# Optimization experiments

Hardware: AMD Instinct MI355X
Metric: run time of the kernel (lower is better)

## Reference

```python
import jax, jax.numpy as jnp
import numpy as np

N_NODES = 50000
N_EDGES = 800000
N_GRAPHS = 64
NEG_SLOPE = 0.2


def _gat_layer(x, src, dst, W, a_src, a_dst, b, heads, out_ch):
    """PyG-style GATConv (concat=True, eval mode, self loops already in src/dst)."""
    N = x.shape[0]
    h = (x @ W).reshape(N, heads, out_ch)                 # [N,H,C]
    al_src = jnp.sum(h * a_src, axis=-1)                  # [N,H]
    al_dst = jnp.sum(h * a_dst, axis=-1)                  # [N,H]
    e = jax.nn.leaky_relu(al_src[src] + al_dst[dst], NEG_SLOPE)  # [E,H]
    m = jax.ops.segment_max(e, dst, num_segments=N)       # scatter-softmax (stable)
    e = jnp.exp(e - m[dst])
    s = jax.ops.segment_sum(e, dst, num_segments=N)
    alpha = e / (s[dst] + 1e-16)                          # [E,H]
    msg = h[src] * alpha[..., None]                       # [E,H,C]
    out = jax.ops.segment_sum(msg, dst, num_segments=N)   # [N,H,C]
    return out.reshape(N, heads * out_ch) + b


def setup_inputs() -> dict:
    key = jax.random.key(0)
    ks = jax.random.split(key, 20)
    x = jax.random.normal(ks[0], (N_NODES, 2), dtype=jnp.float32)
    edge_index = jax.random.randint(ks[1], (2, N_EDGES), 0, N_NODES, dtype=jnp.int64)
    batch = jnp.sort(jax.random.randint(ks[2], (N_NODES,), 0, N_GRAPHS, dtype=jnp.int64))

    def glorot(k, shape):
        fan = sum(shape)
        return jax.random.uniform(k, shape, jnp.float32, -1.0, 1.0) * jnp.sqrt(6.0 / fan)

    return {
        "x": x, "edge_index": edge_index, "batch": batch,
        # gat1: 2 -> 64, heads=2, concat -> 128
        "w1": glorot(ks[3], (2, 128)),
        "a_src1": glorot(ks[4], (2, 64)),
        "a_dst1": glorot(ks[5], (2, 64)),
        "b1": jnp.zeros((128,), jnp.float32),
        # gat2: 128 -> 64, heads=1
        "w2": glorot(ks[6], (128, 64)),
        "a_src2": glorot(ks[7], (1, 64)),
        "a_dst2": glorot(ks[8], (1, 64)),
        "b2": jnp.zeros((64,), jnp.float32),
        # gat3: 64 -> 64, heads=1
        "w3": glorot(ks[9], (64, 64)),
        "a_src3": glorot(ks[10], (1, 64)),
        "a_dst3": glorot(ks[11], (1, 64)),
        "b3": jnp.zeros((64,), jnp.float32),
        # MLP head
        "fw1": glorot(ks[12], (64, 32)),
        "fb1": jnp.zeros((32,), jnp.float32),
        "fw2": glorot(ks[13], (32, 1)),
        "fb2": jnp.zeros((1,), jnp.float32),
    }


def reference(x, edge_index, batch,
              w1, a_src1, a_dst1, b1,
              w2, a_src2, a_dst2, b2,
              w3, a_src3, a_dst3, b3,
              fw1, fb1, fw2, fb2):
    N = x.shape[0]
    loops = jnp.arange(N, dtype=edge_index.dtype)
    src = jnp.concatenate([edge_index[0], loops])  # add self loops (PyG default)
    dst = jnp.concatenate([edge_index[1], loops])

    h = jax.nn.elu(_gat_layer(x, src, dst, w1, a_src1, a_dst1, b1, heads=2, out_ch=64))
    h = jax.nn.elu(_gat_layer(h, src, dst, w2, a_src2, a_dst2, b2, heads=1, out_ch=64))
    h = jax.nn.elu(_gat_layer(h, src, dst, w3, a_src3, a_dst3, b3, heads=1, out_ch=64))

    # global mean pool
    sums = jax.ops.segment_sum(h, batch, num_segments=N_GRAPHS)          # [B,64]
    cnts = jax.ops.segment_sum(jnp.ones((N,), h.dtype), batch, num_segments=N_GRAPHS)
    g = sums / jnp.maximum(cnts, 1.0)[:, None]

    g = jax.nn.relu(g @ fw1 + fb1)
    return g @ fw2 + fb2
```

## Files before the change

kernel.cpp:

```cpp
#include <hip/hip_runtime.h>
#include <hip/hip_bf16.h>
#include <math.h>

#define NN 50000
#define NE 800000
#define ET 850000
#define NG 64
#define NBLK 196


__global__ void count_k(const int* __restrict__ ei, int* __restrict__ counts) {
    int e = blockIdx.x * blockDim.x + threadIdx.x;
    if (e >= ET) return;
    int dst = (e < NE) ? ei[NE + e] : (e - NE);
    atomicAdd(&counts[dst], 1);
}

__global__ __launch_bounds__(256) void scan1_k(const int* __restrict__ counts,
                                               int* __restrict__ offsets,
                                               int* __restrict__ bsum) {
    int t = threadIdx.x;
    int idx = blockIdx.x * 256 + t;
    int v = (idx < NN) ? counts[idx] : 0;
    int lane = t & 63, wave = t >> 6;
    int inc = v;
#pragma unroll
    for (int d = 1; d < 64; d <<= 1) {
        int u = __shfl_up(inc, d);
        if (lane >= d) inc += u;
    }
    __shared__ int wtot[4];
    if (lane == 63) wtot[wave] = inc;
    __syncthreads();
    int wpre = 0;
    for (int w = 0; w < wave; w++) wpre += wtot[w];
    if (idx < NN) offsets[idx] = wpre + inc - v;
    if (t == 255) bsum[blockIdx.x] = wpre + inc;
}

__global__ __launch_bounds__(256) void scan2_k(const int* __restrict__ bsum,
                                               int* __restrict__ bpre,
                                               int* __restrict__ offsets) {
    int t = threadIdx.x;
    int v = (t < NBLK) ? bsum[t] : 0;
    int lane = t & 63, wave = t >> 6;
    int inc = v;
#pragma unroll
    for (int d = 1; d < 64; d <<= 1) {
        int u = __shfl_up(inc, d);
        if (lane >= d) inc += u;
    }
    __shared__ int wtot[4];
    if (lane == 63) wtot[wave] = inc;
    __syncthreads();
    int wpre = 0;
    for (int w = 0; w < wave; w++) wpre += wtot[w];
    if (t < NBLK) bpre[t] = wpre + inc - v;
    if (t == 0) offsets[NN] = ET;
}

__global__ __launch_bounds__(256) void scan3_k(int* __restrict__ offsets,
                                               const int* __restrict__ bpre) {
    int idx = blockIdx.x * 256 + threadIdx.x;
    if (idx < NN) offsets[idx] += bpre[blockIdx.x];
}

__global__ void scatter_k(const int* __restrict__ ei, const int* __restrict__ offsets,
                          int* __restrict__ cursor, int* __restrict__ csr_src) {
    int e = blockIdx.x * blockDim.x + threadIdx.x;
    if (e >= ET) return;
    int src, dst;
    if (e < NE) { src = ei[e]; dst = ei[NE + e]; }
    else        { src = dst = e - NE; }
    int pos = offsets[dst] + atomicAdd(&cursor[dst], 1);
    csr_src[pos] = src;
}

__global__ __launch_bounds__(256) void sortw_k(const int* __restrict__ offsets,
                                               int* __restrict__ csr) {
    int gt = blockIdx.x * blockDim.x + threadIdx.x;
    int n = gt >> 6;
    int lane = gt & 63;
    if (n >= NN) return;
    int b0 = offsets[n], b1 = offsets[n + 1];
    int deg = b1 - b0;
    if (deg <= 1) return;
    if (deg <= 64) {
        int v = (lane < deg) ? csr[b0 + lane] : 0x7FFFFFFF;
#pragma unroll
        for (int k = 2; k <= 64; k <<= 1) {
#pragma unroll
            for (int j = k >> 1; j > 0; j >>= 1) {
                int partner = __shfl_xor(v, j);
                bool up = ((lane & k) == 0);
                bool keepmin = (((lane & j) == 0) == up);
                v = keepmin ? min(v, partner) : max(v, partner);
            }
        }
        if (lane < deg) csr[b0 + lane] = v;
    } else if (lane == 0) {
        for (int i = b0 + 1; i < b1; i++) {
            int v = csr[i];
            int j = i - 1;
            while (j >= b0 && csr[j] > v) { csr[j + 1] = csr[j]; j--; }
            csr[j + 1] = v;
        }
    }
}


__global__ __launch_bounds__(256) void feat1b_k(const float* __restrict__ x,
                                                const float* __restrict__ w1,
                                                const float* __restrict__ as1,
                                                const float* __restrict__ ad1,
                                                float* __restrict__ alS,
                                                float* __restrict__ alD) {
    int t = threadIdx.x;
    int tt = t & 127;
    int n = blockIdx.x * 2 + (t >> 7);
    float x0 = x[n * 2 + 0], x1 = x[n * 2 + 1];
    float v = x0 * w1[tt] + x1 * w1[128 + tt];
    int head = (t >> 6) & 1, lane = t & 63;
    float ps = v * as1[tt];
    float pd = v * ad1[tt];
    for (int d = 32; d; d >>= 1) {
        ps += __shfl_down(ps, d);
        pd += __shfl_down(pd, d);
    }
    if (lane == 0) {
        alS[n * 2 + head] = ps;
        alD[n * 2 + head] = pd;
    }
}


__global__ __launch_bounds__(256) void agg1_k(const float2* __restrict__ x2,
                                              const float* __restrict__ w1,
                                              const float* __restrict__ alS,
                                              const float* __restrict__ alD,
                                              const float* __restrict__ bias,
                                              const int* __restrict__ offsets,
                                              const int* __restrict__ csr,
                                              float* __restrict__ out) {
    __shared__ float4 wslds[4][64];
    int t = threadIdx.x;
    int wave = t >> 6, lane = t & 63, grp = lane >> 4, c4 = lane & 15;
    int gl = lane & 15;
    int n = blockIdx.x * 4 + wave;
    int b0 = offsets[n], b1 = offsets[n + 1];
    int deg = b1 - b0;
    float2 adv = ((const float2*)alD)[n];
    const float2* alS2 = (const float2*)alS;

    float4 wa0 = ((const float4*)w1)[c4];
    float4 wa1 = ((const float4*)w1)[16 + c4];
    float4 wb0 = ((const float4*)(w1 + 128))[c4];
    float4 wb1 = ((const float4*)(w1 + 128))[16 + c4];
    float4 acc0 = make_float4(0.f, 0.f, 0.f, 0.f);
    float4 acc1 = make_float4(0.f, 0.f, 0.f, 0.f);
    float inv0, inv1;

    if (deg <= 64) {
        bool valid = lane < deg;
        int s = 0; float ev0 = -1e30f, ev1 = -1e30f;
        if (valid) {
            s = csr[b0 + lane];
            float2 al = alS2[s];
            float e0 = al.x + adv.x;
            ev0 = e0 > 0.f ? e0 : 0.2f * e0;
            float e1 = al.y + adv.y;
            ev1 = e1 > 0.f ? e1 : 0.2f * e1;
        }
        float m0 = ev0, m1 = ev1;
#pragma unroll
        for (int d = 32; d; d >>= 1) {
            m0 = fmaxf(m0, __shfl_xor(m0, d));
            m1 = fmaxf(m1, __shfl_xor(m1, d));
        }
        if (valid) {
            float w0 = expf(ev0 - m0);
            float w1v = expf(ev1 - m1);
            wslds[wave][lane] = make_float4(w0, w1v, __int_as_float(s), 0.f);
        }
        float ssum0 = 0.f, ssum1 = 0.f;
#pragma unroll
        for (int k = 0; k < 4; k++) {
            int j = gl + 16 * k;
            if (j < deg) {
                float4 f = wslds[wave][j];
                ssum0 += f.x;
                ssum1 += f.y;
            }
        }
        for (int d = 8; d; d >>= 1) {
            ssum0 += __shfl_xor(ssum0, d);
            ssum1 += __shfl_xor(ssum1, d);
        }
        inv0 = 1.f / (ssum0 + 1e-16f);
        inv1 = 1.f / (ssum1 + 1e-16f);
        int j = grp;
        for (; j + 4 < deg; j += 8) {
            float4 fa = wslds[wave][j];
            float4 fb = wslds[wave][j + 4];
            float2 xa = x2[__float_as_int(fa.z)];
            float2 xb = x2[__float_as_int(fb.z)];
            float4 v0, v1;
            v0.x = xa.x * wa0.x + xa.y * wb0.x;
            v0.y = xa.x * wa0.y + xa.y * wb0.y;
            v0.z = xa.x * wa0.z + xa.y * wb0.z;
            v0.w = xa.x * wa0.w + xa.y * wb0.w;
            v1.x = xa.x * wa1.x + xa.y * wb1.x;
            v1.y = xa.x * wa1.y + xa.y * wb1.y;
            v1.z = xa.x * wa1.z + xa.y * wb1.z;
            v1.w = xa.x * wa1.w + xa.y * wb1.w;
            acc0.x = fmaf(fa.x, v0.x, acc0.x);
            acc0.y = fmaf(fa.x, v0.y, acc0.y);
            acc0.z = fmaf(fa.x, v0.z, acc0.z);
            acc0.w = fmaf(fa.x, v0.w, acc0.w);
            acc1.x = fmaf(fa.y, v1.x, acc1.x);
            acc1.y = fmaf(fa.y, v1.y, acc1.y);
            acc1.z = fmaf(fa.y, v1.z, acc1.z);
            acc1.w = fmaf(fa.y, v1.w, acc1.w);
            v0.x = xb.x * wa0.x + xb.y * wb0.x;
            v0.y = xb.x * wa0.y + xb.y * wb0.y;
            v0.z = xb.x * wa0.z + xb.y * wb0.z;
            v0.w = xb.x * wa0.w + xb.y * wb0.w;
            v1.x = xb.x * wa1.x + xb.y * wb1.x;
            v1.y = xb.x * wa1.y + xb.y * wb1.y;
            v1.z = xb.x * wa1.z + xb.y * wb1.z;
            v1.w = xb.x * wa1.w + xb.y * wb1.w;
            acc0.x = fmaf(fb.x, v0.x, acc0.x);
            acc0.y = fmaf(fb.x, v0.y, acc0.y);
            acc0.z = fmaf(fb.x, v0.z, acc0.z);
            acc0.w = fmaf(fb.x, v0.w, acc0.w);
            acc1.x = fmaf(fb.y, v1.x, acc1.x);
            acc1.y = fmaf(fb.y, v1.y, acc1.y);
            acc1.z = fmaf(fb.y, v1.z, acc1.z);
            acc1.w = fmaf(fb.y, v1.w, acc1.w);
        }
        if (j < deg) {
            float4 fa = wslds[wave][j];
            float2 xa = x2[__float_as_int(fa.z)];
            float4 v0, v1;
            v0.x = xa.x * wa0.x + xa.y * wb0.x;
            v0.y = xa.x * wa0.y + xa.y * wb0.y;
            v0.z = xa.x * wa0.z + xa.y * wb0.z;
            v0.w = xa.x * wa0.w + xa.y * wb0.w;
            v1.x = xa.x * wa1.x + xa.y * wb1.x;
            v1.y = xa.x * wa1.y + xa.y * wb1.y;
            v1.z = xa.x * wa1.z + xa.y * wb1.z;
            v1.w = xa.x * wa1.w + xa.y * wb1.w;
            acc0.x = fmaf(fa.x, v0.x, acc0.x);
            acc0.y = fmaf(fa.x, v0.y, acc0.y);
            acc0.z = fmaf(fa.x, v0.z, acc0.z);
            acc0.w = fmaf(fa.x, v0.w, acc0.w);
            acc1.x = fmaf(fa.y, v1.x, acc1.x);
            acc1.y = fmaf(fa.y, v1.y, acc1.y);
            acc1.z = fmaf(fa.y, v1.z, acc1.z);
            acc1.w = fmaf(fa.y, v1.w, acc1.w);
        }
    } else {
        for (int head = 0; head < 2; head++) {
            float ad = head ? adv.y : adv.x;
            float4 wa = head ? wa1 : wa0, wb = head ? wb1 : wb0;
            float m = -1e30f;
            for (int i = b0 + gl; i < b1; i += 16) {
                int s = csr[i];
                float ev = alS[s * 2 + head] + ad;
                ev = ev > 0.f ? ev : 0.2f * ev;
                m = fmaxf(m, ev);
            }
            for (int d = 8; d; d >>= 1) m = fmaxf(m, __shfl_xor(m, d));
            float ssum = 0.f;
            for (int i = b0 + gl; i < b1; i += 16) {
                int s = csr[i];
                float ev = alS[s * 2 + head] + ad;
                ev = ev > 0.f ? ev : 0.2f * ev;
                float w = expf(ev - m);
                ssum += w;
            }
            for (int d = 8; d; d >>= 1) ssum += __shfl_xor(ssum, d);
            float invh = 1.f / (ssum + 1e-16f);
            float4 acc = make_float4(0.f, 0.f, 0.f, 0.f);
            for (int i = b0 + grp; i < b1; i += 4) {
                int s = csr[i];
                float ev = alS[s * 2 + head] + ad;
                ev = ev > 0.f ? ev : 0.2f * ev;
                float w = expf(ev - m);
                float2 xs = x2[s];
                float4 v;
                v.x = xs.x * wa.x + xs.y * wb.x;
                v.y = xs.x * wa.y + xs.y * wb.y;
                v.z = xs.x * wa.z + xs.y * wb.z;
                v.w = xs.x * wa.w + xs.y * wb.w;
                acc.x = fmaf(w, v.x, acc.x);
                acc.y = fmaf(w, v.y, acc.y);
                acc.z = fmaf(w, v.z, acc.z);
                acc.w = fmaf(w, v.w, acc.w);
            }
            if (head == 0) { acc0 = acc; inv0 = invh; }
            else           { acc1 = acc; inv1 = invh; }
        }
    }
#pragma unroll
    for (int mask = 16; mask <= 32; mask <<= 1) {
        acc0.x += __shfl_xor(acc0.x, mask);
        acc0.y += __shfl_xor(acc0.y, mask);
        acc0.z += __shfl_xor(acc0.z, mask);
        acc0.w += __shfl_xor(acc0.w, mask);
        acc1.x += __shfl_xor(acc1.x, mask);
        acc1.y += __shfl_xor(acc1.y, mask);
        acc1.z += __shfl_xor(acc1.z, mask);
        acc1.w += __shfl_xor(acc1.w, mask);
    }
    if (grp < 2) {
        float4 acc = (grp == 0) ? acc0 : acc1;
        float inv = (grp == 0) ? inv0 : inv1;
        float4 b = ((const float4*)bias)[grp * 16 + c4];
        float4 r;
        r.x = acc.x * inv + b.x;
        r.y = acc.y * inv + b.y;
        r.z = acc.z * inv + b.z;
        r.w = acc.w * inv + b.w;
        r.x = r.x > 0.f ? r.x : expm1f(r.x);
        r.y = r.y > 0.f ? r.y : expm1f(r.y);
        r.z = r.z > 0.f ? r.z : expm1f(r.z);
        r.w = r.w > 0.f ? r.w : expm1f(r.w);
        ((float4*)out)[((size_t)n * 2 + grp) * 16 + c4] = r;
    }
}


template <int K>
__global__ __launch_bounds__(256) void gemm_al_k(const float* __restrict__ in,
                                                 const float* __restrict__ W,
                                                 const float* __restrict__ as,
                                                 const float* __restrict__ ad,
                                                 float* __restrict__ h,
                                                 float* __restrict__ alS,
                                                 float* __restrict__ alD) {
    __shared__ float Wl[K * 64];
    __shared__ float rowb[16][K];
    int t = threadIdx.x;
    for (int i = t; i < K * 64; i += 256) Wl[i] = W[i];
    int wave = t >> 6, c = t & 63;
    int nb = blockIdx.x * 16 + wave * 4;
#pragma unroll
    for (int r = 0; r < 4; r++) {
        const float* row = in + (size_t)(nb + r) * K;
        for (int k = c; k < K; k += 64) rowb[wave * 4 + r][k] = row[k];
    }
    __syncthreads();
    const float* rb0 = rowb[wave * 4 + 0];
    const float* rb1 = rowb[wave * 4 + 1];
    const float* rb2 = rowb[wave * 4 + 2];
    const float* rb3 = rowb[wave * 4 + 3];
    float a0 = 0.f, a1 = 0.f, a2 = 0.f, a3 = 0.f;
#pragma unroll 4
    for (int k = 0; k < K; k++) {
        float wv = Wl[k * 64 + c];
        a0 = fmaf(rb0[k], wv, a0);
        a1 = fmaf(rb1[k], wv, a1);
        a2 = fmaf(rb2[k], wv, a2);
        a3 = fmaf(rb3[k], wv, a3);
    }
    h[(size_t)(nb + 0) * 64 + c] = a0;
    h[(size_t)(nb + 1) * 64 + c] = a1;
    h[(size_t)(nb + 2) * 64 + c] = a2;
    h[(size_t)(nb + 3) * 64 + c] = a3;
    float asc = as[c], adc = ad[c];
    float ps0 = a0 * asc, pd0 = a0 * adc;
    float ps1 = a1 * asc, pd1 = a1 * adc;
    float ps2 = a2 * asc, pd2 = a2 * adc;
    float ps3 = a3 * asc, pd3 = a3 * adc;
    for (int d = 32; d; d >>= 1) {
        ps0 += __shfl_down(ps0, d); pd0 += __shfl_down(pd0, d);
        ps1 += __shfl_down(ps1, d); pd1 += __shfl_down(pd1, d);
        ps2 += __shfl_down(ps2, d); pd2 += __shfl_down(pd2, d);
        ps3 += __shfl_down(ps3, d); pd3 += __shfl_down(pd3, d);
    }
    if (c == 0) {
        alS[nb + 0] = ps0; alD[nb + 0] = pd0;
        alS[nb + 1] = ps1; alD[nb + 1] = pd1;
        alS[nb + 2] = ps2; alD[nb + 2] = pd2;
        alS[nb + 3] = ps3; alD[nb + 3] = pd3;
    }
}


__global__ __launch_bounds__(256) void aggf2_k(const float4* __restrict__ h4,
                                               const float* __restrict__ alS,
                                               const float* __restrict__ alD,
                                               const float* __restrict__ bias,
                                               const int* __restrict__ offsets,
                                               const int* __restrict__ csr,
                                               float* __restrict__ out) {
    __shared__ float2 wlds[4][64];
    int t = threadIdx.x;
    int wave = t >> 6, lane = t & 63, grp = lane >> 4, c4 = lane & 15;
    int gl = lane & 15;
    int n = blockIdx.x * 4 + wave;
    int b0 = offsets[n], b1 = offsets[n + 1];
    int deg = b1 - b0;
    float adn = alD[n];

    float4 acc = make_float4(0.f, 0.f, 0.f, 0.f);
    float inv;

    if (deg <= 64) {
        bool valid = lane < deg;
        int s = 0; float ev = -1e30f;
        if (valid) {
            s = csr[b0 + lane];
            float e0 = alS[s] + adn;
            ev = e0 > 0.f ? e0 : 0.2f * e0;
        }
        float m = ev;
#pragma unroll
        for (int d = 32; d; d >>= 1) m = fmaxf(m, __shfl_xor(m, d));
        if (valid) {
            float w = expf(ev - m);
            wlds[wave][lane] = make_float2(w, __int_as_float(s));
        }
        float ssum = 0.f;
#pragma unroll
        for (int k = 0; k < 4; k++) {
            int j = gl + 16 * k;
            if (j < deg) ssum += wlds[wave][j].x;
        }
        for (int d = 8; d; d >>= 1) ssum += __shfl_xor(ssum, d);
        inv = 1.f / (ssum + 1e-16f);
        int j = grp;
        for (; j + 12 < deg; j += 16) {
            float2 f0 = wlds[wave][j];
            float2 f1 = wlds[wave][j + 4];
            float2 f2 = wlds[wave][j + 8];
            float2 f3 = wlds[wave][j + 12];
            float4 v0 = h4[(size_t)__float_as_int(f0.y) * 16 + c4];
            float4 v1 = h4[(size_t)__float_as_int(f1.y) * 16 + c4];
            float4 v2 = h4[(size_t)__float_as_int(f2.y) * 16 + c4];
            float4 v3 = h4[(size_t)__float_as_int(f3.y) * 16 + c4];
            acc.x = fmaf(f0.x, v0.x, acc.x);
            acc.y = fmaf(f0.x, v0.y, acc.y);
            acc.z = fmaf(f0.x, v0.z, acc.z);
            acc.w = fmaf(f0.x, v0.w, acc.w);
            acc.x = fmaf(f1.x, v1.x, acc.x);
            acc.y = fmaf(f1.x, v1.y, acc.y);
            acc.z = fmaf(f1.x, v1.z, acc.z);
            acc.w = fmaf(f1.x, v1.w, acc.w);
            acc.x = fmaf(f2.x, v2.x, acc.x);
            acc.y = fmaf(f2.x, v2.y, acc.y);
            acc.z = fmaf(f2.x, v2.z, acc.z);
            acc.w = fmaf(f2.x, v2.w, acc.w);
            acc.x = fmaf(f3.x, v3.x, acc.x);
            acc.y = fmaf(f3.x, v3.y, acc.y);
            acc.z = fmaf(f3.x, v3.z, acc.z);
            acc.w = fmaf(f3.x, v3.w, acc.w);
        }
        for (; j < deg; j += 4) {
            float2 f0 = wlds[wave][j];
            float4 v0 = h4[(size_t)__float_as_int(f0.y) * 16 + c4];
            acc.x = fmaf(f0.x, v0.x, acc.x);
            acc.y = fmaf(f0.x, v0.y, acc.y);
            acc.z = fmaf(f0.x, v0.z, acc.z);
            acc.w = fmaf(f0.x, v0.w, acc.w);
        }
    } else {
        float m = -1e30f;
        for (int i = b0 + gl; i < b1; i += 16) {
            int s = csr[i];
            float ev = alS[s] + adn;
            ev = ev > 0.f ? ev : 0.2f * ev;
            m = fmaxf(m, ev);
        }
        for (int d = 8; d; d >>= 1) m = fmaxf(m, __shfl_xor(m, d));
        float ssum = 0.f;
        for (int i = b0 + gl; i < b1; i += 16) {
            int s = csr[i];
            float ev = alS[s] + adn;
            ev = ev > 0.f ? ev : 0.2f * ev;
            float w = expf(ev - m);
            ssum += w;
        }
        for (int d = 8; d; d >>= 1) ssum += __shfl_xor(ssum, d);
        inv = 1.f / (ssum + 1e-16f);
        for (int i = b0 + grp; i < b1; i += 4) {
            int s = csr[i];
            float ev = alS[s] + adn;
            ev = ev > 0.f ? ev : 0.2f * ev;
            float w = expf(ev - m);
            float4 v = h4[(size_t)s * 16 + c4];
            acc.x = fmaf(w, v.x, acc.x);
            acc.y = fmaf(w, v.y, acc.y);
            acc.z = fmaf(w, v.z, acc.z);
            acc.w = fmaf(w, v.w, acc.w);
        }
    }
#pragma unroll
    for (int mask = 16; mask <= 32; mask <<= 1) {
        acc.x += __shfl_xor(acc.x, mask);
        acc.y += __shfl_xor(acc.y, mask);
        acc.z += __shfl_xor(acc.z, mask);
        acc.w += __shfl_xor(acc.w, mask);
    }
    if (grp == 0) {
        float4 b = ((const float4*)bias)[c4];
        float4 r;
        r.x = acc.x * inv + b.x;
        r.y = acc.y * inv + b.y;
        r.z = acc.z * inv + b.z;
        r.w = acc.w * inv + b.w;
        r.x = r.x > 0.f ? r.x : expm1f(r.x);
        r.y = r.y > 0.f ? r.y : expm1f(r.y);
        r.z = r.z > 0.f ? r.z : expm1f(r.z);
        r.w = r.w > 0.f ? r.w : expm1f(r.w);
        ((float4*)out)[(size_t)n * 16 + c4] = r;
    }
}


__global__ __launch_bounds__(1024) void pool_k(const float* __restrict__ h,
                                               const int* __restrict__ batch,
                                               float* __restrict__ gout) {
    int g = blockIdx.x;
    __shared__ int sb, se;
    __shared__ float partial[16][64];
    int t = threadIdx.x, wave = t >> 6, c = t & 63;
    if (t == 0) {
        int lo = 0, hi = NN;
        while (lo < hi) { int mid = (lo + hi) >> 1; if (batch[mid] < g) lo = mid + 1; else hi = mid; }
        sb = lo;
        lo = 0; hi = NN;
        while (lo < hi) { int mid = (lo + hi) >> 1; if (batch[mid] < g + 1) lo = mid + 1; else hi = mid; }
        se = lo;
    }
    __syncthreads();
    float acc = 0.f;
    for (int r = sb + wave; r < se; r += 16) acc += h[(size_t)r * 64 + c];
    partial[wave][c] = acc;
    __syncthreads();
    if (wave == 0) {
        float s = 0.f;
#pragma unroll
        for (int wv = 0; wv < 16; wv++) s += partial[wv][c];
        int cnt = se - sb;
        gout[g * 64 + c] = s / fmaxf((float)cnt, 1.0f);
    }
}


__global__ __launch_bounds__(64) void mlp_k(const float* __restrict__ g,
                                            const float* __restrict__ fw1,
                                            const float* __restrict__ fb1,
                                            const float* __restrict__ fw2,
                                            const float* __restrict__ fb2,
                                            float* __restrict__ out) {
    int gi = blockIdx.x;
    __shared__ float gv[64];
    __shared__ float hid[32];
    int t = threadIdx.x;
    gv[t] = g[gi * 64 + t];
    __syncthreads();
    if (t < 32) {
        float a = fb1[t];
        for (int c = 0; c < 64; c++) a += gv[c] * fw1[c * 32 + t];
        hid[t] = a > 0.f ? a : 0.f;
    }
    __syncthreads();
    if (t == 0) {
        float o = fb2[0];
        for (int j = 0; j < 32; j++) o += hid[j] * fw2[j];
        out[gi] = o;
    }
}


extern "C" void kernel_launch(void* const* d_in, const int* in_sizes, int n_in,
                              void* d_out, int out_size, void* d_ws, size_t ws_size,
                              hipStream_t stream) {
    const float* x   = (const float*)d_in[0];
    const int*   ei  = (const int*)d_in[1];
    const int*   bat = (const int*)d_in[2];
    const float* w1  = (const float*)d_in[3];
    const float* as1 = (const float*)d_in[4];
    const float* ad1 = (const float*)d_in[5];
    const float* b1  = (const float*)d_in[6];
    const float* w2  = (const float*)d_in[7];
    const float* as2 = (const float*)d_in[8];
    const float* ad2 = (const float*)d_in[9];
    const float* b2  = (const float*)d_in[10];
    const float* w3  = (const float*)d_in[11];
    const float* as3 = (const float*)d_in[12];
    const float* ad3 = (const float*)d_in[13];
    const float* b3  = (const float*)d_in[14];
    const float* fw1 = (const float*)d_in[15];
    const float* fb1 = (const float*)d_in[16];
    const float* fw2 = (const float*)d_in[17];
    const float* fb2 = (const float*)d_in[18];
    float* out = (float*)d_out;

    char* ws = (char*)d_ws;
    size_t o = 0;
    auto alloc = [&](size_t bytes) -> void* {
        void* p = ws + o;
        o += (bytes + 255) & ~(size_t)255;
        return p;
    };
    int*    counts  = (int*)alloc((NN + 1) * sizeof(int));
    int*    offsets = (int*)alloc((NN + 1) * sizeof(int));
    int*    cursor  = (int*)alloc(NN * sizeof(int));
    int*    bsum    = (int*)alloc(NBLK * sizeof(int));
    int*    bpre    = (int*)alloc(NBLK * sizeof(int));
    int*    csr     = (int*)alloc(ET * sizeof(int));
    float*  l1out   = (float*)alloc((size_t)NN * 128 * sizeof(float));
    float*  hX      = (float*)alloc((size_t)NN * 64 * sizeof(float));
    float*  l2out   = (float*)alloc((size_t)NN * 64 * sizeof(float));
    float*  l3out   = (float*)alloc((size_t)NN * 64 * sizeof(float));
    float*  alS     = (float*)alloc((size_t)NN * 2 * sizeof(float));
    float*  alD     = (float*)alloc((size_t)NN * 2 * sizeof(float));
    float*  gbuf    = (float*)alloc((size_t)NG * 64 * sizeof(float));

    hipMemsetAsync(counts, 0, NN * sizeof(int), stream);
    hipMemsetAsync(cursor, 0, NN * sizeof(int), stream);

    count_k<<<(ET + 255) / 256, 256, 0, stream>>>(ei, counts);
    scan1_k<<<NBLK, 256, 0, stream>>>(counts, offsets, bsum);
    scan2_k<<<1, 256, 0, stream>>>(bsum, bpre, offsets);
    scan3_k<<<NBLK, 256, 0, stream>>>(offsets, bpre);
    scatter_k<<<(ET + 255) / 256, 256, 0, stream>>>(ei, offsets, cursor, csr);
    sortw_k<<<NN / 4, 256, 0, stream>>>(offsets, csr);

    feat1b_k<<<NN / 2, 256, 0, stream>>>(x, w1, as1, ad1, alS, alD);
    agg1_k<<<NN / 4, 256, 0, stream>>>((const float2*)x, w1, alS, alD, b1, offsets, csr, l1out);

    gemm_al_k<128><<<NN / 16, 256, 0, stream>>>(l1out, w2, as2, ad2, hX, alS, alD);
    aggf2_k<<<NN / 4, 256, 0, stream>>>((const float4*)hX, alS, alD, b2, offsets, csr, l2out);

    gemm_al_k<64><<<NN / 16, 256, 0, stream>>>(l2out, w3, as3, ad3, hX, alS, alD);
    aggf2_k<<<NN / 4, 256, 0, stream>>>((const float4*)hX, alS, alD, b3, offsets, csr, l3out);

    pool_k<<<NG, 1024, 0, stream>>>(l3out, bat, gbuf);
    mlp_k<<<NG, 64, 0, stream>>>(gbuf, fw1, fb1, fw2, fb2, out);
}
```

Baseline: 326.8 us.

## Build CSR via two-pass bucketed partition with shared-memory atomics

Replaces the global-atomic count/scatter CSR construction with a bucket partition: per-chunk LDS histograms over 125 destination buckets, a scan of the chunk-by-bucket table, a partition pass that writes packed (local dst, src) words, and a per-bucket kernel that counts, scans and scatters into the CSR using LDS atomics. It removes heavy contended global atomics and the two memsets, at the cost of an extra 850K-entry buffer pass and low parallelism (104 and 125 blocks). The packing assumes src fits in 17 bits.

```diff
diff --git a/kernel.cpp b/kernel.cpp
--- a/kernel.cpp
+++ b/kernel.cpp
@@ -6,22 +6,37 @@
 #define NE 800000
 #define ET 850000
 #define NG 64
-#define NBLK 196
-
-
-__global__ void count_k(const int* __restrict__ ei, int* __restrict__ counts) {
-    int e = blockIdx.x * blockDim.x + threadIdx.x;
-    if (e >= ET) return;
-    int dst = (e < NE) ? ei[NE + e] : (e - NE);
-    atomicAdd(&counts[dst], 1);
-}
-
-__global__ __launch_bounds__(256) void scan1_k(const int* __restrict__ counts,
-                                               int* __restrict__ offsets,
-                                               int* __restrict__ bsum) {
+
+#define NBUK 125
+#define BS   400
+#define CHK  8192
+#define NCH  104
+#define NHIST (NBUK * NCH)
+#define NSB  ((NHIST + 255) / 256)
+
+
+__global__ __launch_bounds__(256) void hist_k(const int* __restrict__ ei,
+                                              int* __restrict__ ghist) {
+    __shared__ int h[NBUK];
+    int c = blockIdx.x, t = threadIdx.x;
+    for (int i = t; i < NBUK; i += 256) h[i] = 0;
+    __syncthreads();
+    int e0 = c * CHK;
+    int e1 = min(ET, e0 + CHK);
+    for (int e = e0 + t; e < e1; e += 256) {
+        int dst = (e < NE) ? ei[NE + e] : (e - NE);
+        atomicAdd(&h[dst / BS], 1);
+    }
+    __syncthreads();
+    for (int b = t; b < NBUK; b += 256) ghist[b * NCH + c] = h[b];
+}
+
+__global__ __launch_bounds__(256) void gscan1_k(const int* __restrict__ in,
+                                                int* __restrict__ out,
+                                                int* __restrict__ bsum, int n) {
     int t = threadIdx.x;
     int idx = blockIdx.x * 256 + t;
-    int v = (idx < NN) ? counts[idx] : 0;
+    int v = (idx < n) ? in[idx] : 0;
     int lane = t & 63, wave = t >> 6;
     int inc = v;
 #pragma unroll
@@ -34,15 +49,15 @@
     __syncthreads();
     int wpre = 0;
     for (int w = 0; w < wave; w++) wpre += wtot[w];
-    if (idx < NN) offsets[idx] = wpre + inc - v;
+    if (idx < n) out[idx] = wpre + inc - v;
     if (t == 255) bsum[blockIdx.x] = wpre + inc;
 }
 
-__global__ __launch_bounds__(256) void scan2_k(const int* __restrict__ bsum,
-                                               int* __restrict__ bpre,
-                                               int* __restrict__ offsets) {
+__global__ __launch_bounds__(256) void gscan2_k(const int* __restrict__ bsum,
+                                                int* __restrict__ bpre, int nb,
+                                                int* __restrict__ tailp, int tailv) {
     int t = threadIdx.x;
-    int v = (t < NBLK) ? bsum[t] : 0;
+    int v = (t < nb) ? bsum[t] : 0;
     int lane = t & 63, wave = t >> 6;
     int inc = v;
 #pragma unroll
@@ -55,25 +70,83 @@
     __syncthreads();
     int wpre = 0;
     for (int w = 0; w < wave; w++) wpre += wtot[w];
-    if (t < NBLK) bpre[t] = wpre + inc - v;
-    if (t == 0) offsets[NN] = ET;
-}
-
-__global__ __launch_bounds__(256) void scan3_k(int* __restrict__ offsets,
-                                               const int* __restrict__ bpre) {
+    if (t < nb) bpre[t] = wpre + inc - v;
+    if (t == 0 && tailp) *tailp = tailv;
+}
+
+__global__ __launch_bounds__(256) void gscan3_k(int* __restrict__ out,
+                                                const int* __restrict__ bpre, int n) {
     int idx = blockIdx.x * 256 + threadIdx.x;
-    if (idx < NN) offsets[idx] += bpre[blockIdx.x];
-}
-
-__global__ void scatter_k(const int* __restrict__ ei, const int* __restrict__ offsets,
-                          int* __restrict__ cursor, int* __restrict__ csr_src) {
-    int e = blockIdx.x * blockDim.x + threadIdx.x;
-    if (e >= ET) return;
-    int src, dst;
-    if (e < NE) { src = ei[e]; dst = ei[NE + e]; }
-    else        { src = dst = e - NE; }
-    int pos = offsets[dst] + atomicAdd(&cursor[dst], 1);
-    csr_src[pos] = src;
+    if (idx < n) out[idx] += bpre[blockIdx.x];
+}
+
+__global__ __launch_bounds__(256) void part_k(const int* __restrict__ ei,
+                                              const int* __restrict__ gbase,
+                                              int* __restrict__ packed) {
+    __shared__ int cur[NBUK];
+    __shared__ int baseL[NBUK];
+    int c = blockIdx.x, t = threadIdx.x;
+    for (int i = t; i < NBUK; i += 256) {
+        cur[i] = 0;
+        baseL[i] = gbase[i * NCH + c];
+    }
+    __syncthreads();
+    int e0 = c * CHK;
+    int e1 = min(ET, e0 + CHK);
+    for (int e = e0 + t; e < e1; e += 256) {
+        int src, dst;
+        if (e < NE) { src = ei[e]; dst = ei[NE + e]; }
+        else        { src = dst = e - NE; }
+        int b = dst / BS;
+        int r = atomicAdd(&cur[b], 1);
+        packed[baseL[b] + r] = ((dst - b * BS) << 17) | src;
+    }
+}
+
+__global__ __launch_bounds__(256) void csr_k(const int* __restrict__ packed,
+                                             const int* __restrict__ gbase,
+                                             int* __restrict__ csr,
+                                             int* __restrict__ offsets) {
+    __shared__ int cnt[BS];
+    __shared__ int sc[2][512];
+    __shared__ int cur[BS];
+    __shared__ int Ss, Ts;
+    int b = blockIdx.x, t = threadIdx.x;
+    for (int i = t; i < BS; i += 256) cnt[i] = 0;
+    if (t == 0) {
+        Ss = gbase[b * NCH];
+        Ts = (b == NBUK - 1) ? ET : gbase[(b + 1) * NCH];
+    }
+    __syncthreads();
+    int n0 = Ss, n1 = Ts;
+    for (int i = n0 + t; i < n1; i += 256) {
+        int p = packed[i];
+        atomicAdd(&cnt[p >> 17], 1);
+    }
+    __syncthreads();
+    for (int i = t; i < 512; i += 256) sc[0][i] = (i < BS) ? cnt[i] : 0;
+    __syncthreads();
+    int pp = 0;
+    for (int d = 1; d < 512; d <<= 1) {
+        for (int i = t; i < 512; i += 256) {
+            int v = sc[pp][i];
+            if (i >= d) v += sc[pp][i - d];
+            sc[pp ^ 1][i] = v;
+        }
+        pp ^= 1;
+        __syncthreads();
+    }
+    for (int i = t; i < BS; i += 256) {
+        int pre = (i == 0) ? 0 : sc[pp][i - 1];
+        offsets[b * BS + i] = Ss + pre;
+        cur[i] = Ss + pre;
+    }
+    __syncthreads();
+    for (int i = n0 + t; i < n1; i += 256) {
+        int p = packed[i];
+        int pos = atomicAdd(&cur[p >> 17], 1);
+        csr[pos] = p & 0x1FFFF;
+    }
 }
 
 __global__ __launch_bounds__(256) void sortw_k(const int* __restrict__ offsets,
@@ -606,11 +679,12 @@
         o += (bytes + 255) & ~(size_t)255;
         return p;
     };
-    int*    counts  = (int*)alloc((NN + 1) * sizeof(int));
     int*    offsets = (int*)alloc((NN + 1) * sizeof(int));
-    int*    cursor  = (int*)alloc(NN * sizeof(int));
-    int*    bsum    = (int*)alloc(NBLK * sizeof(int));
-    int*    bpre    = (int*)alloc(NBLK * sizeof(int));
+    int*    ghist   = (int*)alloc(NHIST * sizeof(int));
+    int*    gbase   = (int*)alloc(NHIST * sizeof(int));
+    int*    bsum    = (int*)alloc(NSB * sizeof(int));
+    int*    bpre    = (int*)alloc(NSB * sizeof(int));
+    int*    packed  = (int*)alloc(ET * sizeof(int));
     int*    csr     = (int*)alloc(ET * sizeof(int));
     float*  l1out   = (float*)alloc((size_t)NN * 128 * sizeof(float));
     float*  hX      = (float*)alloc((size_t)NN * 64 * sizeof(float));
@@ -620,14 +694,12 @@
     float*  alD     = (float*)alloc((size_t)NN * 2 * sizeof(float));
     float*  gbuf    = (float*)alloc((size_t)NG * 64 * sizeof(float));
 
-    hipMemsetAsync(counts, 0, NN * sizeof(int), stream);
-    hipMemsetAsync(cursor, 0, NN * sizeof(int), stream);
-
-    count_k<<<(ET + 255) / 256, 256, 0, stream>>>(ei, counts);
-    scan1_k<<<NBLK, 256, 0, stream>>>(counts, offsets, bsum);
-    scan2_k<<<1, 256, 0, stream>>>(bsum, bpre, offsets);
-    scan3_k<<<NBLK, 256, 0, stream>>>(offsets, bpre);
-    scatter_k<<<(ET + 255) / 256, 256, 0, stream>>>(ei, offsets, cursor, csr);
+    hist_k<<<NCH, 256, 0, stream>>>(ei, ghist);
+    gscan1_k<<<NSB, 256, 0, stream>>>(ghist, gbase, bsum, NHIST);
+    gscan2_k<<<1, 256, 0, stream>>>(bsum, bpre, NSB, offsets + NN, ET);
+    gscan3_k<<<NSB, 256, 0, stream>>>(gbase, bpre, NHIST);
+    part_k<<<NCH, 256, 0, stream>>>(ei, gbase, packed);
+    csr_k<<<NBUK, 256, 0, stream>>>(packed, gbase, csr, offsets);
     sortw_k<<<NN / 4, 256, 0, stream>>>(offsets, csr);
 
     feat1b_k<<<NN / 2, 256, 0, stream>>>(x, w1, as1, ad1, alS, alD);
```

Result: faster. 280.5 us, median of 2 (-14.2%).
